# Kernel tuning notes

Hardware: AMD Instinct MI355X
Metric: run time of the kernel (lower is better)

Reference implementation:

```python
import jax, jax.numpy as jnp
import numpy as np

V = 200000  # num entities
R = 100     # num relations
D = 128     # embedding_dim
K = 20      # entity_neighbor_num
B = 128     # batch (docs)
N = 50      # entities per doc


def setup_inputs() -> dict:
    key = jax.random.key(0)
    ks = jax.random.split(key, 8)
    return {
        "entity_ids": jax.random.randint(ks[0], (B, N), 0, V),
        "adj_entity": jax.random.randint(ks[1], (V, K), 0, V),
        "adj_relation": jax.random.randint(ks[2], (V, K), 0, R),
        "entity_embedding": jax.random.normal(ks[3], (V, D), jnp.float32),
        "relation_embedding": jax.random.normal(ks[4], (R, D), jnp.float32),
        "W_att": jax.random.normal(ks[5], (3 * D, 1), jnp.float32) * 0.05,
        "b_att": jnp.zeros((1,), jnp.float32),
        "W_conv": jax.random.normal(ks[6], (2 * D, D), jnp.float32) * 0.05,
        "b_conv": jnp.zeros((D,), jnp.float32),
    }


def reference(entity_ids, adj_entity, adj_relation, entity_embedding,
              relation_embedding, W_att, b_att, W_conv, b_conv):
    # neighbor ids: [B, N, K]
    neigh_ent = adj_entity[entity_ids]
    neigh_rel = adj_relation[entity_ids]
    ne = entity_embedding[neigh_ent]      # [B, N, K, D]
    nr = relation_embedding[neigh_rel]    # [B, N, K, D]
    ee = entity_embedding[entity_ids]     # [B, N, D]
    ee_exp = jnp.broadcast_to(ee[:, :, None, :], ne.shape)  # [B, N, K, D]
    concat = jnp.concatenate([ee_exp, ne, nr], axis=-1)     # [B, N, K, 3D]
    logits = jax.nn.relu(concat @ W_att + b_att)            # [B, N, K, 1]
    # NOTE: faithful to original nn.Softmax(dim=0) -> softmax over batch axis
    att = jax.nn.softmax(logits, axis=0)                    # [B, N, K, 1]
    neighbor_att = jnp.sum(att * ne, axis=2)                # [B, N, D]
    agg_in = jnp.concatenate([ee, neighbor_att], axis=-1)   # [B, N, 2D]
    return jax.nn.relu(agg_in @ W_conv + b_conv)            # [B, N, D]
```

## Files before the change

### kernel.cpp

```cpp
#include <hip/hip_runtime.h>

#define V 200000
#define R 100
#define D 128
#define K 20
#define B 128
#define N 50

__global__ void k_rel_score(const float* __restrict__ RE,
                            const float* __restrict__ Watt,
                            float* __restrict__ rel_score) {
  __shared__ float red[128];
  const int r = blockIdx.x;
  const int t = threadIdx.x;
  red[t] = RE[r * D + t] * Watt[2 * D + t];
  __syncthreads();
  for (int s = 64; s > 0; s >>= 1) {
    if (t < s) red[t] += red[t + s];
    __syncthreads();
  }
  if (t == 0) rel_score[r] = red[0];
}

__global__ void k_logits(const int* __restrict__ eids,
                         const int* __restrict__ adjE,
                         const int* __restrict__ adjR,
                         const float* __restrict__ EE,
                         const float* __restrict__ Watt,
                         const float* __restrict__ batt,
                         const float* __restrict__ rel_score,
                         float* __restrict__ att) {
  const int bn = blockIdx.x;
  const int b = bn / N;
  const int n = bn % N;
  const int lane = threadIdx.x;
  const int eid = eids[bn];

  const float2 wa_e = ((const float2*)Watt)[lane];
  const float2 wa_n = ((const float2*)(Watt + D))[lane];

  const float2 e2 = ((const float2*)(EE + (size_t)eid * D))[lane];
  float p = e2.x * wa_e.x + e2.y * wa_e.y;
  #pragma unroll
  for (int off = 32; off > 0; off >>= 1) p += __shfl_down(p, off);
  const float s_ee = __shfl(p, 0) + batt[0];

  const int* ae = adjE + (size_t)eid * K;
  const int* ar = adjR + (size_t)eid * K;

  for (int k = 0; k < K; ++k) {
    const int nid = ae[k];
    const int rid = ar[k];
    const float2 ne2 = ((const float2*)(EE + (size_t)nid * D))[lane];
    float q = ne2.x * wa_n.x + ne2.y * wa_n.y;
    #pragma unroll
    for (int off = 32; off > 0; off >>= 1) q += __shfl_down(q, off);
    if (lane == 0) {
      float logit = s_ee + q + rel_score[rid];
      att[(n * K + k) * B + b] = logit > 0.0f ? logit : 0.0f;
    }
  }
}

__global__ void k_softmax(float* __restrict__ att) {
  __shared__ float red[4];
  const int g = blockIdx.x;
  const int t = threadIdx.x;
  const float x = att[g * B + t];

  float m = x;
  #pragma unroll
  for (int off = 32; off > 0; off >>= 1) m = fmaxf(m, __shfl_down(m, off));
  if ((t & 63) == 0) red[t >> 6] = m;
  __syncthreads();
  const float mm = fmaxf(red[0], red[1]);

  const float e = __expf(x - mm);
  float s = e;
  #pragma unroll
  for (int off = 32; off > 0; off >>= 1) s += __shfl_down(s, off);
  if ((t & 63) == 0) red[2 + (t >> 6)] = s;
  __syncthreads();
  const float ss = red[2] + red[3];

  att[g * B + t] = e / ss;
}

#define G 4
__global__ void k_out(const int* __restrict__ eids,
                      const int* __restrict__ adjE,
                      const float* __restrict__ EE,
                      const float* __restrict__ att,
                      const float* __restrict__ Wc,
                      const float* __restrict__ bc,
                      float* __restrict__ out) {
  __shared__ float agg[G][2 * D];
  __shared__ float s_att[G][K];
  __shared__ int   s_nid[G][K];

  const int d = threadIdx.x;
  const int base = blockIdx.x * G;

  for (int j = 0; j < G; ++j) {
    const int bn = base + j;
    const int b = bn / N;
    const int n = bn % N;
    const int eid = eids[bn];
    if (d < K) {
      s_nid[j][d] = adjE[(size_t)eid * K + d];
      s_att[j][d] = att[(n * K + d) * B + b];
    }
  }
  __syncthreads();

  for (int j = 0; j < G; ++j) {
    const int bn = base + j;
    const int eid = eids[bn];
    const float ee = EE[(size_t)eid * D + d];
    float na = 0.0f;
    #pragma unroll
    for (int k = 0; k < K; ++k)
      na += s_att[j][k] * EE[(size_t)s_nid[j][k] * D + d];
    agg[j][d] = ee;
    agg[j][D + d] = na;
  }
  __syncthreads();

  float acc[G];
  #pragma unroll
  for (int j = 0; j < G; ++j) acc[j] = 0.0f;
  for (int i = 0; i < 2 * D; ++i) {
    const float w = Wc[i * D + d];
    #pragma unroll
    for (int j = 0; j < G; ++j) acc[j] += agg[j][i] * w;
  }
  const float bb = bc[d];
  for (int j = 0; j < G; ++j) {
    const float v = acc[j] + bb;
    out[(size_t)(base + j) * D + d] = v > 0.0f ? v : 0.0f;
  }
}

extern "C" void kernel_launch(void* const* d_in, const int* in_sizes, int n_in,
                              void* d_out, int out_size, void* d_ws, size_t ws_size,
                              hipStream_t stream) {
  const int*   eids = (const int*)d_in[0];
  const int*   adjE = (const int*)d_in[1];
  const int*   adjR = (const int*)d_in[2];
  const float* EE   = (const float*)d_in[3];
  const float* RE   = (const float*)d_in[4];
  const float* Watt = (const float*)d_in[5];
  const float* batt = (const float*)d_in[6];
  const float* Wc   = (const float*)d_in[7];
  const float* bc   = (const float*)d_in[8];
  float* out = (float*)d_out;

  float* att       = (float*)d_ws;
  float* rel_score = att + (size_t)N * K * B;

  k_rel_score<<<R, 128, 0, stream>>>(RE, Watt, rel_score);
  k_logits<<<B * N, 64, 0, stream>>>(eids, adjE, adjR, EE, Watt, batt,
                                     rel_score, att);
  k_softmax<<<N * K, 128, 0, stream>>>(att);
  k_out<<<(B * N) / G, 128, 0, stream>>>(eids, adjE, EE, att, Wc, bc, out);
}
```

Before: 213.8 us.

## Fuse relation scoring into logits kernel and split output GEMV across half-blocks

Removes the separate relation-score kernel by computing the relation dot product inline from the relation embedding inside the logits kernel. In that kernel each wavefront now splits into four 16-lane groups that handle different neighbors with float4 loads and short shuffles, and four entity positions share a 256-thread block. The output kernel uses 256 threads, splitting the aggregation and the 2D-by-D matvec reduction across two halves and combining the halves through shared memory. This cuts one launch and the serial per-neighbor full-wave reductions, at the cost of rereading relation rows per neighbor and an extra shared-memory reduction step.

```diff
diff --git a/kernel.cpp b/kernel.cpp
--- a/kernel.cpp
+++ b/kernel.cpp
@@ -7,56 +7,62 @@
 #define B 128
 #define N 50
 
-__global__ void k_rel_score(const float* __restrict__ RE,
-                            const float* __restrict__ Watt,
-                            float* __restrict__ rel_score) {
-  __shared__ float red[128];
-  const int r = blockIdx.x;
-  const int t = threadIdx.x;
-  red[t] = RE[r * D + t] * Watt[2 * D + t];
-  __syncthreads();
-  for (int s = 64; s > 0; s >>= 1) {
-    if (t < s) red[t] += red[t + s];
-    __syncthreads();
-  }
-  if (t == 0) rel_score[r] = red[0];
-}
-
 __global__ void k_logits(const int* __restrict__ eids,
                          const int* __restrict__ adjE,
                          const int* __restrict__ adjR,
                          const float* __restrict__ EE,
+                         const float* __restrict__ RE,
                          const float* __restrict__ Watt,
                          const float* __restrict__ batt,
-                         const float* __restrict__ rel_score,
                          float* __restrict__ att) {
-  const int bn = blockIdx.x;
+  const int lane = threadIdx.x & 63;
+  const int wv   = threadIdx.x >> 6;
+  const int bn   = blockIdx.x * 4 + wv;
   const int b = bn / N;
   const int n = bn % N;
-  const int lane = threadIdx.x;
   const int eid = eids[bn];
 
   const float2 wa_e = ((const float2*)Watt)[lane];
-  const float2 wa_n = ((const float2*)(Watt + D))[lane];
-
-  const float2 e2 = ((const float2*)(EE + (size_t)eid * D))[lane];
+  const float2 e2   = ((const float2*)(EE + (size_t)eid * D))[lane];
   float p = e2.x * wa_e.x + e2.y * wa_e.y;
   #pragma unroll
   for (int off = 32; off > 0; off >>= 1) p += __shfl_down(p, off);
   const float s_ee = __shfl(p, 0) + batt[0];
 
-  const int* ae = adjE + (size_t)eid * K;
-  const int* ar = adjR + (size_t)eid * K;
+  const int g  = lane >> 4;
+  const int sl = lane & 15;
+  const float4* wnp = (const float4*)(Watt + D + 8 * sl);
+  const float4* wrp = (const float4*)(Watt + 2 * D + 8 * sl);
+  const float4 wn0 = wnp[0], wn1 = wnp[1];
+  const float4 wr0 = wrp[0], wr1 = wrp[1];
 
-  for (int k = 0; k < K; ++k) {
+  const int* ae = adjE + eid * K;
+  const int* ar = adjR + eid * K;
+
+  float q[5];
+  #pragma unroll
+  for (int k5 = 0; k5 < 5; ++k5) {
+    const int k = k5 * 4 + g;
     const int nid = ae[k];
     const int rid = ar[k];
-    const float2 ne2 = ((const float2*)(EE + (size_t)nid * D))[lane];
-    float q = ne2.x * wa_n.x + ne2.y * wa_n.y;
+    const float4* np = (const float4*)(EE + (size_t)nid * D + 8 * sl);
+    const float4* rp = (const float4*)(RE + (size_t)rid * D + 8 * sl);
+    const float4 n0 = np[0], n1 = np[1];
+    const float4 r0 = rp[0], r1 = rp[1];
+    float s = n0.x * wn0.x + n0.y * wn0.y + n0.z * wn0.z + n0.w * wn0.w
+            + n1.x * wn1.x + n1.y * wn1.y + n1.z * wn1.z + n1.w * wn1.w
+            + r0.x * wr0.x + r0.y * wr0.y + r0.z * wr0.z + r0.w * wr0.w
+            + r1.x * wr1.x + r1.y * wr1.y + r1.z * wr1.z + r1.w * wr1.w;
     #pragma unroll
-    for (int off = 32; off > 0; off >>= 1) q += __shfl_down(q, off);
-    if (lane == 0) {
-      float logit = s_ee + q + rel_score[rid];
+    for (int off = 8; off > 0; off >>= 1) s += __shfl_down(s, off, 16);
+    q[k5] = s;
+  }
+
+  if (sl == 0) {
+    #pragma unroll
+    for (int k5 = 0; k5 < 5; ++k5) {
+      const int k = k5 * 4 + g;
+      const float logit = s_ee + q[k5];
       att[(n * K + k) * B + b] = logit > 0.0f ? logit : 0.0f;
     }
   }
@@ -64,9 +70,9 @@
 
 __global__ void k_softmax(float* __restrict__ att) {
   __shared__ float red[4];
-  const int g = blockIdx.x;
+  const int gg = blockIdx.x;
   const int t = threadIdx.x;
-  const float x = att[g * B + t];
+  const float x = att[gg * B + t];
 
   float m = x;
   #pragma unroll
@@ -83,7 +89,7 @@
   __syncthreads();
   const float ss = red[2] + red[3];
 
-  att[g * B + t] = e / ss;
+  att[gg * B + t] = e / ss;
 }
 
 #define G 4
@@ -95,25 +101,29 @@
                       const float* __restrict__ bc,
                       float* __restrict__ out) {
   __shared__ float agg[G][2 * D];
+  __shared__ float part[2][G][D];
   __shared__ float s_att[G][K];
   __shared__ int   s_nid[G][K];
 
-  const int d = threadIdx.x;
+  const int t = threadIdx.x;
+  const int d = t & 127;
+  const int h = t >> 7;
   const int base = blockIdx.x * G;
 
-  for (int j = 0; j < G; ++j) {
+  if (t < G * K) {
+    const int j = t / K, k = t % K;
     const int bn = base + j;
     const int b = bn / N;
     const int n = bn % N;
     const int eid = eids[bn];
-    if (d < K) {
-      s_nid[j][d] = adjE[(size_t)eid * K + d];
-      s_att[j][d] = att[(n * K + d) * B + b];
-    }
+    s_nid[j][k] = adjE[eid * K + k];
+    s_att[j][k] = att[(n * K + k) * B + b];
   }
   __syncthreads();
 
-  for (int j = 0; j < G; ++j) {
+  #pragma unroll
+  for (int jj = 0; jj < 2; ++jj) {
+    const int j = h + jj * 2;
     const int bn = base + j;
     const int eid = eids[bn];
     const float ee = EE[(size_t)eid * D + d];
@@ -126,17 +136,35 @@
   }
   __syncthreads();
 
-  float acc[G];
+  float acc0 = 0.f, acc1 = 0.f, acc2 = 0.f, acc3 = 0.f;
+  const int ibase = h * D;
+  #pragma unroll 4
+  for (int c = 0; c < 32; ++c) {
+    const int i = ibase + c * 4;
+    const float4 a0 = *(const float4*)&agg[0][i];
+    const float4 a1 = *(const float4*)&agg[1][i];
+    const float4 a2 = *(const float4*)&agg[2][i];
+    const float4 a3 = *(const float4*)&agg[3][i];
+    const float w0 = Wc[(i + 0) * D + d];
+    const float w1 = Wc[(i + 1) * D + d];
+    const float w2 = Wc[(i + 2) * D + d];
+    const float w3 = Wc[(i + 3) * D + d];
+    acc0 += a0.x * w0 + a0.y * w1 + a0.z * w2 + a0.w * w3;
+    acc1 += a1.x * w0 + a1.y * w1 + a1.z * w2 + a1.w * w3;
+    acc2 += a2.x * w0 + a2.y * w1 + a2.z * w2 + a2.w * w3;
+    acc3 += a3.x * w0 + a3.y * w1 + a3.z * w2 + a3.w * w3;
+  }
+  part[h][0][d] = acc0;
+  part[h][1][d] = acc1;
+  part[h][2][d] = acc2;
+  part[h][3][d] = acc3;
+  __syncthreads();
+
+  const float bb = bc[d];
   #pragma unroll
-  for (int j = 0; j < G; ++j) acc[j] = 0.0f;
-  for (int i = 0; i < 2 * D; ++i) {
-    const float w = Wc[i * D + d];
-    #pragma unroll
-    for (int j = 0; j < G; ++j) acc[j] += agg[j][i] * w;
-  }
-  const float bb = bc[d];
-  for (int j = 0; j < G; ++j) {
-    const float v = acc[j] + bb;
+  for (int jj = 0; jj < 2; ++jj) {
+    const int j = h + jj * 2;
+    const float v = part[0][j][d] + part[1][j][d] + bb;
     out[(size_t)(base + j) * D + d] = v > 0.0f ? v : 0.0f;
   }
 }
@@ -155,12 +183,10 @@
   const float* bc   = (const float*)d_in[8];
   float* out = (float*)d_out;
 
-  float* att       = (float*)d_ws;
-  float* rel_score = att + (size_t)N * K * B;
+  float* att = (float*)d_ws;
 
-  k_rel_score<<<R, 128, 0, stream>>>(RE, Watt, rel_score);
-  k_logits<<<B * N, 64, 0, stream>>>(eids, adjE, adjR, EE, Watt, batt,
-                                     rel_score, att);
+  k_logits<<<(B * N) / 4, 256, 0, stream>>>(eids, adjE, adjR, EE, RE, Watt,
+                                            batt, att);
   k_softmax<<<N * K, 128, 0, stream>>>(att);
-  k_out<<<(B * N) / G, 128, 0, stream>>>(eids, adjE, EE, att, Wc, bc, out);
+  k_out<<<(B * N) / G, 256, 0, stream>>>(eids, adjE, EE, att, Wc, bc, out);
 }
```

Measured after the change: 213.3 us. About the same (-0.2%).
